# Kernel optimization log

Measured on AMD Instinct MI355X. Metric: run time of the kernel, lower is better.

Reference implementation:

```python
import jax, jax.numpy as jnp
import numpy as np
from jax import lax

B, N, C, NP, NS, H, L = 2, 16384, 256, 2048, 32, 4, 2
DFF = 2 * C
RADIUS = 1.0
EPS = 1e-5


def setup_inputs() -> dict:
    key = jax.random.key(0)
    ks = jax.random.split(key, 12)
    s = 0.02
    f32 = jnp.float32
    return {
        "xyz": jax.random.normal(ks[0], (B, N, 3), f32),
        "features": jax.random.normal(ks[1], (B, C, N), f32),
        # positional encoding: Conv1x1(3->C/2)+BN(eval)+ReLU, Conv1x1(C/2->C)
        "pe1_w": jax.random.normal(ks[2], (C // 2, 3), f32) * s,
        "pe1_b": jnp.zeros((C // 2,), f32),
        "bn_g": jnp.ones((C // 2,), f32),
        "bn_b": jnp.zeros((C // 2,), f32),
        "bn_m": jnp.zeros((C // 2,), f32),
        "bn_v": jnp.ones((C // 2,), f32),
        "pe2_w": jax.random.normal(ks[3], (C, C // 2), f32) * s,
        "pe2_b": jnp.zeros((C,), f32),
        # L pre-norm transformer encoder layers (stacked on leading dim)
        "ipw": jax.random.normal(ks[4], (L, 3 * C, C), f32) * s,
        "ipb": jnp.zeros((L, 3 * C), f32),
        "opw": jax.random.normal(ks[5], (L, C, C), f32) * s,
        "opb": jnp.zeros((L, C), f32),
        "ln1s": jnp.ones((L, C), f32), "ln1b": jnp.zeros((L, C), f32),
        "ln2s": jnp.ones((L, C), f32), "ln2b": jnp.zeros((L, C), f32),
        "fc1w": jax.random.normal(ks[6], (L, DFF, C), f32) * s,
        "fc1b": jnp.zeros((L, DFF), f32),
        "fc2w": jax.random.normal(ks[7], (L, C, DFF), f32) * s,
        "fc2b": jnp.zeros((L, C), f32),
    }


def _fps(xyz, npoint):
    # D-FPS starting from point 0 (pointnet2 convention). xyz: [B,N,3]
    b, n, _ = xyz.shape

    def step(carry, _):
        dists, far = carry
        centroid = jnp.take_along_axis(xyz, far[:, None, None], axis=1)  # [B,1,3]
        d = jnp.sum((xyz - centroid) ** 2, -1)
        dists = jnp.minimum(dists, d)
        return (dists, jnp.argmax(dists, -1).astype(jnp.int32)), far

    init = (jnp.full((b, n), 1e10, jnp.float32), jnp.zeros((b,), jnp.int32))
    _, idx = lax.scan(step, init, None, length=npoint)
    return idx.T  # [B, npoint]


def _ball_query(xyz, new_xyz, radius, ns):
    # first <=ns points within radius, padded with the first hit. [B,NP,NS]
    n = xyz.shape[1]
    d2 = jnp.sum((new_xyz[:, :, None, :] - xyz[:, None, :, :]) ** 2, -1)  # [B,NP,N]
    scores = jnp.where(d2 < radius * radius, jnp.arange(n, dtype=jnp.int32), n)
    svals = jnp.sort(scores, axis=-1)[..., :ns]
    order = jnp.argsort(scores, axis=-1)[..., :ns].astype(jnp.int32)
    valid = svals < n
    return jnp.where(valid, order, order[..., :1])


def _ln(x, s, b):
    m = jnp.mean(x, -1, keepdims=True)
    v = jnp.var(x, -1, keepdims=True)
    return (x - m) * lax.rsqrt(v + EPS) * s + b


def _mha(x, w, bias, ow, ob):
    # x: [S, Bn, D] (seq-first, like nn.MultiheadAttention)
    S, Bn, D = x.shape
    hd = D // H
    qkv = x @ w.T + bias
    q, k, v = jnp.split(qkv, 3, -1)
    rs = lambda t: t.reshape(S, Bn, H, hd).transpose(1, 2, 0, 3)  # [Bn,H,S,hd]
    q, k, v = rs(q), rs(k), rs(v)
    att = jax.nn.softmax(jnp.einsum('bhqd,bhkd->bhqk', q, k) * (1.0 / np.sqrt(hd)), -1)
    o = jnp.einsum('bhqk,bhkd->bhqd', att, v).transpose(2, 0, 1, 3).reshape(S, Bn, D)
    return o @ ow.T + ob


def reference(xyz, features, pe1_w, pe1_b, bn_g, bn_b, bn_m, bn_v, pe2_w, pe2_b,
              ipw, ipb, opw, opb, ln1s, ln1b, ln2s, ln2b, fc1w, fc1b, fc2w, fc2b):
    # --- sample + group ---
    fps_idx = _fps(lax.stop_gradient(xyz), NP)                       # [B,NP]
    new_xyz = jnp.take_along_axis(xyz, fps_idx[:, :, None], axis=1)  # [B,NP,3]
    idx = _ball_query(lax.stop_gradient(xyz), lax.stop_gradient(new_xyz), RADIUS, NS)
    g_xyz = jax.vmap(lambda p, i: p[i])(xyz, idx) - new_xyz[:, :, None, :]  # [B,NP,NS,3]
    g_xyz = g_xyz.transpose(0, 3, 1, 2)                              # [B,3,NP,NS]
    g_feat = jax.vmap(lambda f, i: f[:, i])(features, idx)           # [B,C,NP,NS]
    # --- positional encoding (conv1x1 + BN(eval) + ReLU, conv1x1) ---
    h = jnp.einsum('oc,bcps->bops', pe1_w, g_xyz) + pe1_b[None, :, None, None]
    h = (h - bn_m[None, :, None, None]) * lax.rsqrt(bn_v + EPS)[None, :, None, None]
    h = jax.nn.relu(h * bn_g[None, :, None, None] + bn_b[None, :, None, None])
    pe = jnp.einsum('oc,bcps->bops', pe2_w, h) + pe2_b[None, :, None, None]
    x = g_feat + pe                                                  # [B,C,NP,NS]
    # --- local transformer over each neighborhood (seq len = NS) ---
    x = x.transpose(0, 2, 1, 3).reshape(B * NP, C, NS).transpose(2, 0, 1)  # [NS,B*NP,C]
    for l in range(L):
        x = _ln(x, ln1s[l], ln1b[l])
        x = x + _mha(x, ipw[l], ipb[l], opw[l], opb[l])
        x = _ln(x, ln2s[l], ln2b[l])
        x = x + jax.nn.relu(x @ fc1w[l].T + fc1b[l]) @ fc2w[l].T + fc2b[l]
    tf = x.transpose(1, 2, 0).reshape(B, NP, C, NS).transpose(0, 2, 1, 3)  # [B,C,NP,NS]
    Lf = NP * NS

    def scat(feat_b, tf_b, idx_b):
        idx_f = idx_b.reshape(-1)          # [Lf]
        ff = tf_b.reshape(C, -1)           # [C,Lf]
        pos = jnp.arange(Lf, dtype=jnp.int32)
        first = jax.ops.segment_min(pos, idx_f, num_segments=N)  # [N], maxint if absent
        valid = first < Lf
        safe = jnp.where(valid, first, 0)
        return jnp.where(valid[None, :], ff[:, safe], feat_b)    # [C,N]

    out = jax.vmap(scat)(features, tf, idx)  # [B,C,N]
    return out.transpose(0, 2, 1)            # [B,N,C]
```

## Files before the change

kernel.cpp:

```cpp
#include <hip/hip_runtime.h>

#define NB 2
#define NN 16384
#define NC 256
#define NPp 2048
#define NSs 32
#define NH 4
#define HDh 64
#define NL 2
#define NDFF 512
#define LFv (NPp*NSs)
#define LNEPS 1e-5f
#define NBLK 256
#define NTHR 512

typedef short s16x8 __attribute__((ext_vector_type(8)));
typedef float f32x4 __attribute__((ext_vector_type(4)));
typedef float f32x2 __attribute__((ext_vector_type(2)));
typedef unsigned short u16;
typedef unsigned long long u64;

struct CtlBlock { int prog[2]; int ctr1; int ctr2; int bar; };

__device__ __forceinline__ u16 f2bf(float f){
  unsigned u = __float_as_uint(f);
  u += 0x7fffu + ((u>>16)&1u);
  return (u16)(u>>16);
}

__device__ __forceinline__ f32x4 mfma16(s16x8 a, s16x8 b, f32x4 c){
  return __builtin_amdgcn_mfma_f32_16x16x32_bf16(a, b, c, 0, 0, 0);
}

__device__ __forceinline__ f32x2 pk_add(f32x2 a, f32x2 b){
  f32x2 d; asm("v_pk_add_f32 %0, %1, %2" : "=v"(d) : "v"(a), "v"(b)); return d;
}
__device__ __forceinline__ f32x2 pk_mul(f32x2 a, f32x2 b){
  f32x2 d; asm("v_pk_mul_f32 %0, %1, %2" : "=v"(d) : "v"(a), "v"(b)); return d;
}

#define DPP_FMAX(v, ctrl) do { \
  int _iv = __float_as_int(v); \
  int _sh = __builtin_amdgcn_update_dpp(_iv, _iv, (ctrl), 0xF, 0xF, false); \
  (v) = fmaxf((v), __int_as_float(_sh)); \
} while(0)

#define DPP_IMIN(v, ctrl) do { \
  int _sh = __builtin_amdgcn_update_dpp((v), (v), (ctrl), 0xF, 0xF, false); \
  (v) = (_sh < (v)) ? _sh : (v); \
} while(0)

struct SMem {
  u64  masks[256];
  u64  keybuf[4];
  float xs[32][NC];
  u16  xn[32][264];
  u16  qb[32][776];
  u16  pb[NH][32][40];
  int  idx_sh[32];
  float gx_sh[32][3];
  float wcoord[2][8][4];
  int  misc[16];
  int  win[32];
};

__global__ void k_prep(const float* __restrict__ ipw, const float* __restrict__ opw,
                       const float* __restrict__ fc1w, const float* __restrict__ fc2w,
                       const float* __restrict__ pe2w,
                       const float* __restrict__ bng, const float* __restrict__ bnb,
                       const float* __restrict__ bnm, const float* __restrict__ bnv,
                       u16* ipwb, u16* opwb, u16* fc1wb, u16* fc2wb, u16* pe2wb,
                       float* bnsc, float* bnsh, int* first, CtlBlock* ctl){
  const int i0 = blockIdx.x*blockDim.x + threadIdx.x;
  const int stride = gridDim.x*blockDim.x;
  for (int i=i0; i<NL*768*NC; i+=stride) ipwb[i] = f2bf(ipw[i]);
  for (int i=i0; i<NL*NC*NC; i+=stride)  opwb[i] = f2bf(opw[i]);
  for (int i=i0; i<NL*NDFF*NC; i+=stride) fc1wb[i] = f2bf(fc1w[i]);
  for (int i=i0; i<NL*NC*NDFF; i+=stride) fc2wb[i] = f2bf(fc2w[i]);
  for (int i=i0; i<NC*128; i+=stride)    pe2wb[i] = f2bf(pe2w[i]);
  for (int i=i0; i<NB*NN; i+=stride)     first[i] = LFv;
  for (int i=i0; i<128; i+=stride){
    float sc = bng[i]*rsqrtf(bnv[i]+LNEPS);
    bnsc[i] = sc; bnsh[i] = bnb[i] - bnm[i]*sc;
  }
  if (i0 == 0){
    ctl->prog[0] = -1; ctl->prog[1] = -1;
    ctl->ctr1 = 0; ctl->ctr2 = 0; ctl->bar = 0;
  }
}

__global__ __launch_bounds__(256) void k_featT(const float* __restrict__ feat,
                                               float* __restrict__ featT){
  __shared__ float T[32][33];
  const int b = blockIdx.y;
  const int n0 = blockIdx.x*32;
  const int t = threadIdx.x;
  const int tn = t & 31, tc = t >> 5;
  for (int cb=0; cb<NC; cb+=32){
    #pragma unroll
    for (int i=0;i<32;i+=8)
      T[tc+i][tn] = feat[((size_t)b*NC + cb+tc+i)*NN + n0+tn];
    __syncthreads();
    #pragma unroll
    for (int i=0;i<32;i+=8)
      featT[((size_t)b*NN + n0+tc+i)*NC + cb+tn] = T[tn][tc+i];
    __syncthreads();
  }
}

__device__ void fps_run(int b, const float* __restrict__ xyz,
                        float* __restrict__ newxyz, CtlBlock* ctl, SMem& sm){
#pragma clang fp contract(off)
  const int t = threadIdx.x;
  const int lane = t & 63, wid = t >> 6;
  const float* xb = xyz + (size_t)b*NN*3;
  f32x2 px2[16], py2[16], pz2[16], dd2[16];
  #pragma unroll
  for (int m=0;m<16;m++){
    int i0 = t + (2*m)*NTHR, i1 = t + (2*m+1)*NTHR;
    px2[m] = f32x2{xb[i0*3],   xb[i1*3]};
    py2[m] = f32x2{xb[i0*3+1], xb[i1*3+1]};
    pz2[m] = f32x2{xb[i0*3+2], xb[i1*3+2]};
    dd2[m] = f32x2{1e10f, 1e10f};
  }
  if (t < 4) sm.keybuf[t] = 0ull;
  float wx = xb[0], wy = xb[1], wz = xb[2];
  if (t==0){
    newxyz[(size_t)b*NPp*3+0]=wx;
    newxyz[(size_t)b*NPp*3+1]=wy;
    newxyz[(size_t)b*NPp*3+2]=wz;
    __hip_atomic_store(&ctl->prog[b], 0, __ATOMIC_RELEASE, __HIP_MEMORY_SCOPE_AGENT);
  }
  float ncx=-wx, ncy=-wy, ncz=-wz;
  __syncthreads();
  for (int step=1; step<NPp; ++step){
    const f32x2 ncx2={ncx,ncx}, ncy2={ncy,ncy}, ncz2={ncz,ncz};
    #pragma unroll
    for (int m=0;m<16;m++){
      f32x2 dx = pk_add(px2[m], ncx2);
      f32x2 dy = pk_add(py2[m], ncy2);
      f32x2 dz = pk_add(pz2[m], ncz2);
      f32x2 s  = pk_add(pk_add(pk_mul(dx,dx), pk_mul(dy,dy)), pk_mul(dz,dz));
      f32x2 d  = dd2[m];
      d.x = fminf(d.x, s.x);
      d.y = fminf(d.y, s.y);
      dd2[m] = d;
    }
    float h8[8];
    #pragma unroll
    for (int q=0;q<8;q++)
      h8[q] = fmaxf(fmaxf(dd2[2*q].x, dd2[2*q].y), fmaxf(dd2[2*q+1].x, dd2[2*q+1].y));
    float M = fmaxf(fmaxf(fmaxf(h8[0],h8[1]),fmaxf(h8[2],h8[3])),
                    fmaxf(fmaxf(h8[4],h8[5]),fmaxf(h8[6],h8[7])));
    DPP_FMAX(M, 0x111); DPP_FMAX(M, 0x112); DPP_FMAX(M, 0x114); DPP_FMAX(M, 0x118);
    DPP_FMAX(M, 0x142); DPP_FMAX(M, 0x143);
    const unsigned Mb = (unsigned)__builtin_amdgcn_readlane(__float_as_int(M), 63);
    const float Ms = __int_as_float((int)Mb);
    int li = 0x7fffffff;
    #pragma unroll
    for (int m=15;m>=0;m--){
      if (dd2[m].y == Ms) li = t + (2*m+1)*NTHR;
      if (dd2[m].x == Ms) li = t + (2*m)*NTHR;
    }
    DPP_IMIN(li, 0x111); DPP_IMIN(li, 0x112); DPP_IMIN(li, 0x114); DPP_IMIN(li, 0x118);
    DPP_IMIN(li, 0x142); DPP_IMIN(li, 0x143);
    const int li63 = __builtin_amdgcn_readlane(li, 63);
    const int kb = step & 3, cb = step & 1;
    if (lane==0){
      u64 key = ((u64)Mb << 32) | (unsigned)(0x7fffffff - li63);
      atomicMax(&sm.keybuf[kb], key);
      const float* cp = xb + (size_t)li63*3;
      sm.wcoord[cb][wid][0]=cp[0]; sm.wcoord[cb][wid][1]=cp[1]; sm.wcoord[cb][wid][2]=cp[2];
    }
    __syncthreads();
    const u64 kk = sm.keybuf[kb];
    const int widx = 0x7fffffff - (int)(unsigned)(kk & 0xffffffffu);
    const int wv = (widx & (NTHR-1)) >> 6;
    const float nx = sm.wcoord[cb][wv][0];
    const float ny = sm.wcoord[cb][wv][1];
    const float nz = sm.wcoord[cb][wv][2];
    ncx=-nx; ncy=-ny; ncz=-nz;
    if (t==0){
      newxyz[((size_t)b*NPp+step)*3+0]=nx;
      newxyz[((size_t)b*NPp+step)*3+1]=ny;
      newxyz[((size_t)b*NPp+step)*3+2]=nz;
      sm.keybuf[(step+2)&3] = 0ull;
      if ((step & 7) == 7 || step == NPp-1)
        __hip_atomic_store(&ctl->prog[b], step, __ATOMIC_RELEASE, __HIP_MEMORY_SCOPE_AGENT);
    }
  }
}

__device__ void seq_ballq(const float* __restrict__ xb, float cx, float cy, float cz,
                          SMem& sm, int t, int lane, int wid){
#pragma clang fp contract(off)
  for (int it=0; it<32; ++it){
    int cid = wid*32 + it;
    int i = cid*64 + lane;
    float dx=xb[i*3]-cx, dy=xb[i*3+1]-cy, dz=xb[i*3+2]-cz;
    float d2=(dx*dx+dy*dy)+dz*dz;
    u64 m = __ballot(d2 < 1.0f);
    if (lane==0) sm.masks[cid] = m;
  }
  __syncthreads();
  if (wid==0){
    u64 mk[4]; int cnt=0;
    #pragma unroll
    for (int j=0;j<4;j++){ mk[j]=sm.masks[lane*4+j]; cnt += __popcll(mk[j]); }
    int inc = cnt;
    #pragma unroll
    for (int ofs=1; ofs<64; ofs<<=1){
      int v = __shfl_up(inc, ofs);
      if (lane >= ofs) inc += v;
    }
    int r = inc - cnt;
    int tot = __shfl(inc, 63);
    #pragma unroll
    for (int j=0;j<4;j++){
      u64 msk = mk[j];
      int base = (lane*4+j)*64;
      while (msk && r < NSs){
        int bpos = __ffsll(msk)-1;
        sm.idx_sh[r] = base + bpos;
        msk &= msk-1;
        ++r;
      }
      if (r >= NSs) break;
    }
    int cc = tot < NSs ? tot : NSs;
    int pv = (tot > 0) ? sm.idx_sh[0] : 0;
    if (lane < NSs && lane >= cc) sm.idx_sh[lane] = pv;
  }
  __syncthreads();
}

__device__ __forceinline__ void ln_block512(SMem& sm, const float* __restrict__ s_,
                                            const float* __restrict__ b_, int t){
  const int s = t >> 4, j = t & 15;
  float v[16];
  float sum = 0.f;
  #pragma unroll
  for (int k=0;k<16;k++){ v[k]=sm.xs[s][j*16+k]; sum += v[k]; }
  #pragma unroll
  for (int m=1;m<16;m<<=1) sum += __shfl_xor(sum, m);
  const float mean = sum * (1.f/256.f);
  float vs = 0.f;
  #pragma unroll
  for (int k=0;k<16;k++){ float d=v[k]-mean; vs += d*d; }
  #pragma unroll
  for (int m=1;m<16;m<<=1) vs += __shfl_xor(vs, m);
  const float rstd = rsqrtf(vs*(1.f/256.f) + LNEPS);
  #pragma unroll
  for (int k=0;k<16;k++){
    int c = j*16+k;
    float y = (v[k]-mean)*rstd*s_[c] + b_[c];
    sm.xs[s][c] = y;
    sm.xn[s][c] = f2bf(y);
  }
}

__device__ void seq_pe_tf(SMem& sm, int b, int p,
    const float* __restrict__ xyz, const float* __restrict__ features,
    const float* __restrict__ featT, int useT, const float* __restrict__ newxyz,
    const float* __restrict__ pe1w, const float* __restrict__ pe1b,
    const float* __restrict__ bnsc, const float* __restrict__ bnsh,
    const u16* __restrict__ pe2wb, const float* __restrict__ pe2b,
    const u16* __restrict__ ipwb, const float* __restrict__ ipb,
    const u16* __restrict__ opwb, const float* __restrict__ opb,
    const float* __restrict__ ln1s, const float* __restrict__ ln1b,
    const float* __restrict__ ln2s, const float* __restrict__ ln2b,
    const u16* __restrict__ fc1wb, const float* __restrict__ fc1b,
    const u16* __restrict__ fc2wb, const float* __restrict__ fc2b){
  const int t = threadIdx.x, lane = t & 63, wid = t >> 6;
  const int c15 = lane & 15, g4 = lane >> 4;

  if (t < 96){
    int s = t/3, d = t%3;
    sm.gx_sh[s][d] = xyz[((size_t)b*NN + sm.idx_sh[s])*3 + d] - newxyz[(size_t)p*3 + d];
  }
  if (useT){
    for (int e=t; e<32*NC; e+=NTHR){
      int s=e>>8, c=e&255;
      sm.xs[s][c] = featT[((size_t)b*NN + sm.idx_sh[s])*NC + c];
    }
  } else {
    for (int e=t; e<32*NC; e+=NTHR){
      int s=e>>8, c=e&255;
      sm.xs[s][c] = features[((size_t)b*NC + c)*NN + sm.idx_sh[s]];
    }
  }
  __syncthreads();
  for (int i=t; i<32*128; i+=NTHR){
    int s = i >> 7, o = i & 127;
    float h = pe1w[o*3]*sm.gx_sh[s][0] + pe1w[o*3+1]*sm.gx_sh[s][1] + pe1w[o*3+2]*sm.gx_sh[s][2] + pe1b[o];
    h = h*bnsc[o] + bnsh[o];
    sm.xn[s][o] = f2bf(h > 0.f ? h : 0.f);
  }
  __syncthreads();
  for (int tt=wid; tt<32; tt+=8){
    int m0 = (tt & 1)*16, n0 = (tt >> 1)*16;
    f32x4 acc = {0.f,0.f,0.f,0.f};
    #pragma unroll
    for (int kk=0; kk<4; kk++){
      s16x8 a = *(const s16x8*)&sm.xn[m0+c15][kk*32 + g4*8];
      s16x8 bb = *(const s16x8*)&pe2wb[(size_t)(n0+c15)*128 + kk*32 + g4*8];
      acc = mfma16(a, bb, acc);
    }
    int col = n0 + c15;
    float bias = pe2b[col];
    #pragma unroll
    for (int r=0;r<4;r++) sm.xs[m0 + g4*4 + r][col] += acc[r] + bias;
  }
  __syncthreads();

  for (int l=0; l<NL; ++l){
    ln_block512(sm, ln1s + l*NC, ln1b + l*NC, t);
    __syncthreads();
    const u16* Wq = ipwb + (size_t)l*768*NC;
    const float* bq = ipb + l*768;
    for (int tt=wid; tt<96; tt+=8){
      int m0 = (tt & 1)*16, n0 = (tt >> 1)*16;
      f32x4 acc = {0.f,0.f,0.f,0.f};
      #pragma unroll
      for (int kk=0;kk<8;kk++){
        s16x8 a = *(const s16x8*)&sm.xn[m0+c15][kk*32 + g4*8];
        s16x8 bb = *(const s16x8*)&Wq[(size_t)(n0+c15)*NC + kk*32 + g4*8];
        acc = mfma16(a, bb, acc);
      }
      int col = n0 + c15;
      float bias = bq[col];
      #pragma unroll
      for (int r=0;r<4;r++) sm.qb[m0 + g4*4 + r][col] = f2bf(acc[r] + bias);
    }
    __syncthreads();
    {
      const int h = wid & 3;
      const int mt = wid >> 2;
      f32x4 lac[2];
      #pragma unroll
      for (int nt=0;nt<2;nt++){
        f32x4 acc = {0.f,0.f,0.f,0.f};
        #pragma unroll
        for (int kk=0;kk<2;kk++){
          s16x8 a = *(const s16x8*)&sm.qb[mt*16+c15][h*HDh + kk*32 + g4*8];
          s16x8 bb = *(const s16x8*)&sm.qb[nt*16+c15][256 + h*HDh + kk*32 + g4*8];
          acc = mfma16(a, bb, acc);
        }
        lac[nt] = acc;
      }
      #pragma unroll
      for (int r=0;r<4;r++){
        float v0 = lac[0][r]*0.125f, v1 = lac[1][r]*0.125f;
        float mx = fmaxf(v0, v1);
        #pragma unroll
        for (int m=1;m<16;m<<=1) mx = fmaxf(mx, __shfl_xor(mx, m));
        float e0 = expf(v0-mx), e1 = expf(v1-mx);
        float smm = e0 + e1;
        #pragma unroll
        for (int m=1;m<16;m<<=1) smm += __shfl_xor(smm, m);
        float inv = 1.f/smm;
        int row = mt*16 + g4*4 + r;
        sm.pb[h][row][c15]    = f2bf(e0*inv);
        sm.pb[h][row][16+c15] = f2bf(e1*inv);
      }
      f32x4 oac[4];
      #pragma unroll
      for (int nt=0;nt<4;nt++){
        s16x8 bb;
        #pragma unroll
        for (int e=0;e<8;e++) bb[e] = (short)sm.qb[g4*8+e][512 + h*HDh + nt*16 + c15];
        f32x4 acc = {0.f,0.f,0.f,0.f};
        s16x8 a = *(const s16x8*)&sm.pb[h][mt*16+c15][g4*8];
        oac[nt] = mfma16(a, bb, acc);
      }
      __syncthreads();
      #pragma unroll
      for (int nt=0;nt<4;nt++)
        #pragma unroll
        for (int r=0;r<4;r++)
          sm.xn[mt*16 + g4*4 + r][h*HDh + nt*16 + c15] = f2bf(oac[nt][r]);
    }
    __syncthreads();
    const u16* Wo = opwb + (size_t)l*NC*NC;
    const float* bo = opb + l*NC;
    for (int tt=wid; tt<32; tt+=8){
      int m0 = (tt & 1)*16, n0 = (tt >> 1)*16;
      f32x4 acc = {0.f,0.f,0.f,0.f};
      #pragma unroll
      for (int kk=0;kk<8;kk++){
        s16x8 a = *(const s16x8*)&sm.xn[m0+c15][kk*32 + g4*8];
        s16x8 bb = *(const s16x8*)&Wo[(size_t)(n0+c15)*NC + kk*32 + g4*8];
        acc = mfma16(a, bb, acc);
      }
      int col = n0 + c15;
      float bias = bo[col];
      #pragma unroll
      for (int r=0;r<4;r++) sm.xs[m0 + g4*4 + r][col] += acc[r] + bias;
    }
    __syncthreads();
    ln_block512(sm, ln2s + l*NC, ln2b + l*NC, t);
    __syncthreads();
    const u16* W1 = fc1wb + (size_t)l*NDFF*NC;
    for (int tt=wid; tt<64; tt+=8){
      int m0 = (tt & 1)*16, n0 = (tt >> 1)*16;
      f32x4 acc = {0.f,0.f,0.f,0.f};
      #pragma unroll
      for (int kk=0;kk<8;kk++){
        s16x8 a = *(const s16x8*)&sm.xn[m0+c15][kk*32 + g4*8];
        s16x8 bb = *(const s16x8*)&W1[(size_t)(n0+c15)*NC + kk*32 + g4*8];
        acc = mfma16(a, bb, acc);
      }
      int col = n0 + c15;
      float bias = fc1b[l*NDFF + col];
      #pragma unroll
      for (int r=0;r<4;r++){
        float v = acc[r] + bias;
        sm.qb[m0 + g4*4 + r][col] = f2bf(v > 0.f ? v : 0.f);
      }
    }
    __syncthreads();
    const u16* W2 = fc2wb + (size_t)l*NC*NDFF;
    for (int tt=wid; tt<32; tt+=8){
      int m0 = (tt & 1)*16, n0 = (tt >> 1)*16;
      f32x4 acc = {0.f,0.f,0.f,0.f};
      #pragma unroll
      for (int kk=0;kk<16;kk++){
        s16x8 a = *(const s16x8*)&sm.qb[m0+c15][kk*32 + g4*8];
        s16x8 bb = *(const s16x8*)&W2[(size_t)(n0+c15)*NDFF + kk*32 + g4*8];
        acc = mfma16(a, bb, acc);
      }
      int col = n0 + c15;
      float bias = fc2b[l*NC + col];
      #pragma unroll
      for (int r=0;r<4;r++) sm.xs[m0 + g4*4 + r][col] += acc[r] + bias;
    }
    __syncthreads();
  }
}

__global__ __launch_bounds__(NTHR,1) void k_mega(
    const float* __restrict__ xyz, const float* __restrict__ features,
    const float* __restrict__ featT, int useT,
    float* __restrict__ newxyz, int* __restrict__ first, CtlBlock* ctl,
    const float* __restrict__ pe1w, const float* __restrict__ pe1b,
    const float* __restrict__ bnsc, const float* __restrict__ bnsh,
    const u16* __restrict__ pe2wb, const float* __restrict__ pe2b,
    const u16* __restrict__ ipwb, const float* __restrict__ ipb,
    const u16* __restrict__ opwb, const float* __restrict__ opb,
    const float* __restrict__ ln1s, const float* __restrict__ ln1b,
    const float* __restrict__ ln2s, const float* __restrict__ ln2b,
    const u16* __restrict__ fc1wb, const float* __restrict__ fc1b,
    const u16* __restrict__ fc2wb, const float* __restrict__ fc2b,
    float* __restrict__ out){
  __shared__ SMem sm;
  const int t = threadIdx.x, lane = t & 63, wid = t >> 6;

  if (blockIdx.x < NB){
    fps_run(blockIdx.x, xyz, newxyz, ctl, sm);
  } else {
    for (;;){
      if (t==0) sm.misc[1] = atomicAdd(&ctl->ctr1, 1);
      __syncthreads();
      int p = sm.misc[1];
      if (p >= NB*NPp) break;
      int b = p >> 11, pp = p & (NPp-1);
      if (t==0){
        while (__hip_atomic_load(&ctl->prog[b], __ATOMIC_RELAXED, __HIP_MEMORY_SCOPE_AGENT) < pp)
          __builtin_amdgcn_s_sleep(2);
        __builtin_amdgcn_fence(__ATOMIC_ACQUIRE, "agent");
      }
      __syncthreads();
      float cx = newxyz[(size_t)p*3], cy = newxyz[(size_t)p*3+1], cz = newxyz[(size_t)p*3+2];
      seq_ballq(xyz + (size_t)b*NN*3, cx, cy, cz, sm, t, lane, wid);
      if (t < NSs) atomicMin(&first[b*NN + sm.idx_sh[t]], pp*NSs + t);
      __syncthreads();
    }
  }

  __syncthreads();
  if (t==0){
    __builtin_amdgcn_fence(__ATOMIC_RELEASE, "agent");
    __hip_atomic_fetch_add(&ctl->bar, 1, __ATOMIC_RELAXED, __HIP_MEMORY_SCOPE_AGENT);
    while (__hip_atomic_load(&ctl->bar, __ATOMIC_RELAXED, __HIP_MEMORY_SCOPE_AGENT) < NBLK)
      __builtin_amdgcn_s_sleep(8);
    __builtin_amdgcn_fence(__ATOMIC_ACQUIRE, "agent");
  }
  __syncthreads();

  for (;;){
    if (t==0) sm.misc[1] = atomicAdd(&ctl->ctr2, 1);
    __syncthreads();
    int p = sm.misc[1];
    if (p >= NB*NPp) break;
    int b = p >> 11, pp = p & (NPp-1);
    float cx = newxyz[(size_t)p*3], cy = newxyz[(size_t)p*3+1], cz = newxyz[(size_t)p*3+2];
    seq_ballq(xyz + (size_t)b*NN*3, cx, cy, cz, sm, t, lane, wid);
    if (t==0) sm.misc[2] = 0;
    __syncthreads();
    if (t < NSs){
      int pos = pp*NSs + t;
      int f = __hip_atomic_load(&first[b*NN + sm.idx_sh[t]], __ATOMIC_RELAXED, __HIP_MEMORY_SCOPE_AGENT);
      int w = (f == pos) ? 1 : 0;
      sm.win[t] = w;
      if (w) atomicOr(&sm.misc[2], 1);
    }
    __syncthreads();
    if (!sm.misc[2]) continue;
    seq_pe_tf(sm, b, p, xyz, features, featT, useT, newxyz,
              pe1w, pe1b, bnsc, bnsh, pe2wb, pe2b, ipwb, ipb, opwb, opb,
              ln1s, ln1b, ln2s, ln2b, fc1wb, fc1b, fc2wb, fc2b);
    for (int e=t; e<NSs*NC; e+=NTHR){
      int s = e >> 8, c = e & 255;
      if (sm.win[s]) out[((size_t)b*NN + sm.idx_sh[s])*NC + c] = sm.xs[s][c];
    }
    __syncthreads();
  }
}

__global__ __launch_bounds__(256) void k_outfill_T(const float* __restrict__ featT,
                                                   const int* __restrict__ first,
                                                   float* __restrict__ out){
  const int t = threadIdx.x;
  for (int rr=0; rr<8; ++rr){
    int row = blockIdx.x*8 + rr;
    if (first[row] == LFv)
      out[(size_t)row*NC + t] = featT[(size_t)row*NC + t];
  }
}

__global__ __launch_bounds__(256) void k_outfill_noT(const float* __restrict__ feat,
                                                     const int* __restrict__ first,
                                                     float* __restrict__ out){
  __shared__ float T[32][33];
  const int b = blockIdx.y;
  const int n0 = blockIdx.x*32;
  const int t = threadIdx.x;
  const int tn = t & 31, tc = t >> 5;
  for (int cb=0; cb<NC; cb+=32){
    #pragma unroll
    for (int i=0;i<32;i+=8)
      T[tc+i][tn] = feat[((size_t)b*NC + cb+tc+i)*NN + n0+tn];
    __syncthreads();
    #pragma unroll
    for (int i=0;i<32;i+=8){
      int n = n0 + tc + i;
      if (first[b*NN+n] == LFv)
        out[((size_t)b*NN + n)*NC + cb+tn] = T[tn][tc+i];
    }
    __syncthreads();
  }
}

extern "C" void kernel_launch(void* const* d_in, const int* in_sizes, int n_in,
                              void* d_out, int out_size, void* d_ws, size_t ws_size,
                              hipStream_t stream){
  const float* xyz   = (const float*)d_in[0];
  const float* feat  = (const float*)d_in[1];
  const float* pe1w  = (const float*)d_in[2];
  const float* pe1b  = (const float*)d_in[3];
  const float* bng   = (const float*)d_in[4];
  const float* bnb   = (const float*)d_in[5];
  const float* bnm   = (const float*)d_in[6];
  const float* bnv   = (const float*)d_in[7];
  const float* pe2w  = (const float*)d_in[8];
  const float* pe2b  = (const float*)d_in[9];
  const float* ipw   = (const float*)d_in[10];
  const float* ipb   = (const float*)d_in[11];
  const float* opw   = (const float*)d_in[12];
  const float* opb   = (const float*)d_in[13];
  const float* ln1s  = (const float*)d_in[14];
  const float* ln1b  = (const float*)d_in[15];
  const float* ln2s  = (const float*)d_in[16];
  const float* ln2b  = (const float*)d_in[17];
  const float* fc1w  = (const float*)d_in[18];
  const float* fc1b  = (const float*)d_in[19];
  const float* fc2w  = (const float*)d_in[20];
  const float* fc2b  = (const float*)d_in[21];
  float* out = (float*)d_out;

  char* ws = (char*)d_ws;
  size_t off = 0;
  auto alloc = [&](size_t bytes)->void*{
    void* p = ws + off;
    off = (off + bytes + 255) & ~(size_t)255;
    return p;
  };
  float* newxyz  = (float*)alloc((size_t)NB*NPp*3*4);
  int*   first   = (int*)  alloc((size_t)NB*NN*4);
  CtlBlock* ctl  = (CtlBlock*)alloc(sizeof(CtlBlock));
  float* bnsc    = (float*)alloc(128*4);
  float* bnsh    = (float*)alloc(128*4);
  u16*   ipwb    = (u16*)  alloc((size_t)NL*768*NC*2);
  u16*   opwb    = (u16*)  alloc((size_t)NL*NC*NC*2);
  u16*   fc1wb   = (u16*)  alloc((size_t)NL*NDFF*NC*2);
  u16*   fc2wb   = (u16*)  alloc((size_t)NL*NC*NDFF*2);
  u16*   pe2wb   = (u16*)  alloc((size_t)NC*128*2);
  float* featT   = (float*)(ws + off);
  int useT = (off + (size_t)NB*NN*NC*4 <= ws_size) ? 1 : 0;

  k_prep<<<512, 256, 0, stream>>>(ipw, opw, fc1w, fc2w, pe2w, bng, bnb, bnm, bnv,
                                  ipwb, opwb, fc1wb, fc2wb, pe2wb, bnsc, bnsh, first, ctl);
  if (useT)
    k_featT<<<dim3(NN/32, NB), 256, 0, stream>>>(feat, featT);

  const float* featT_c = featT;
  void* kargs[] = {
    (void*)&xyz, (void*)&feat, (void*)&featT_c, (void*)&useT,
    (void*)&newxyz, (void*)&first, (void*)&ctl,
    (void*)&pe1w, (void*)&pe1b, (void*)&bnsc, (void*)&bnsh,
    (void*)&pe2wb, (void*)&pe2b, (void*)&ipwb, (void*)&ipb,
    (void*)&opwb, (void*)&opb, (void*)&ln1s, (void*)&ln1b,
    (void*)&ln2s, (void*)&ln2b, (void*)&fc1wb, (void*)&fc1b,
    (void*)&fc2wb, (void*)&fc2b, (void*)&out };
  hipLaunchCooperativeKernel((void*)k_mega, dim3(NBLK), dim3(NTHR), kargs, 0, stream);

  if (useT)
    k_outfill_T<<<(NB*NN)/8, 256, 0, stream>>>(featT, first, out);
  else
    k_outfill_noT<<<dim3(NN/32, NB), 256, 0, stream>>>(feat, first, out);
  (void)in_sizes; (void)n_in; (void)out_size;
}
```

Baseline: 4.474 ms.

## Speculatively run neighborhood transformers during FPS and commit winners afterwards

Worker blocks now run the full positional-encoding and transformer pipeline for every neighborhood as soon as its FPS centroid is ready. Each result is stored in a bf16 buffer, and a new commit kernel picks the first-occurrence winner per point or falls back to the input features. This hides the transformer work behind the serial FPS phase instead of running it in a second pass after FPS. The cost is computing every neighborhood rather than only the winners, a large extra workspace, and bf16 rounding of outputs. The FPS step is also reworked: the cross-wave argmax uses per-wave shared-memory keys instead of a shared atomicMax, the winner's coordinates are read from registers, and only indices are stored, with centroid coordinates re-read from xyz.

```diff
diff --git a/kernel.cpp b/kernel.cpp
--- a/kernel.cpp
+++ b/kernel.cpp
@@ -52,14 +52,15 @@
 
 struct SMem {
   u64  masks[256];
-  u64  keybuf[4];
-  float xs[32][NC];
+  u64  wvkey[2][8];
+  float wvc[2][8][4];
+  int  idxbuf[8];
+  float xs[32][260];
   u16  xn[32][264];
   u16  qb[32][776];
   u16  pb[NH][32][40];
   int  idx_sh[32];
   float gx_sh[32][3];
-  float wcoord[2][8][4];
   int  misc[16];
   int  win[32];
 };
@@ -108,8 +109,10 @@
   }
 }
 
-__device__ void fps_run(int b, const float* __restrict__ xyz,
-                        float* __restrict__ newxyz, CtlBlock* ctl, SMem& sm){
+#define SELC(S) case S: scx = px2[(S)>>1][(S)&1]; scy = py2[(S)>>1][(S)&1]; scz = pz2[(S)>>1][(S)&1]; break;
+
+__device__ void fps_run(int b, const float* __restrict__ xyz, int* __restrict__ fps_idx,
+                        CtlBlock* ctl, SMem& sm){
 #pragma clang fp contract(off)
   const int t = threadIdx.x;
   const int lane = t & 63, wid = t >> 6;
@@ -123,15 +126,15 @@
     pz2[m] = f32x2{xb[i0*3+2], xb[i1*3+2]};
     dd2[m] = f32x2{1e10f, 1e10f};
   }
-  if (t < 4) sm.keybuf[t] = 0ull;
-  float wx = xb[0], wy = xb[1], wz = xb[2];
-  if (t==0){
-    newxyz[(size_t)b*NPp*3+0]=wx;
-    newxyz[(size_t)b*NPp*3+1]=wy;
-    newxyz[(size_t)b*NPp*3+2]=wz;
-    __hip_atomic_store(&ctl->prog[b], 0, __ATOMIC_RELEASE, __HIP_MEMORY_SCOPE_AGENT);
-  }
-  float ncx=-wx, ncy=-wy, ncz=-wz;
+  float ncx, ncy, ncz;
+  {
+    float wx = xb[0], wy = xb[1], wz = xb[2];
+    ncx=-wx; ncy=-wy; ncz=-wz;
+    if (t==0){
+      fps_idx[b*NPp] = 0;
+      __hip_atomic_store(&ctl->prog[b], 0, __ATOMIC_RELEASE, __HIP_MEMORY_SCOPE_AGENT);
+    }
+  }
   __syncthreads();
   for (int step=1; step<NPp; ++step){
     const f32x2 ncx2={ncx,ncx}, ncy2={ncy,ncy}, ncz2={ncz,ncz};
@@ -154,8 +157,8 @@
                     fmaxf(fmaxf(h8[4],h8[5]),fmaxf(h8[6],h8[7])));
     DPP_FMAX(M, 0x111); DPP_FMAX(M, 0x112); DPP_FMAX(M, 0x114); DPP_FMAX(M, 0x118);
     DPP_FMAX(M, 0x142); DPP_FMAX(M, 0x143);
-    const unsigned Mb = (unsigned)__builtin_amdgcn_readlane(__float_as_int(M), 63);
-    const float Ms = __int_as_float((int)Mb);
+    const int Mi = __builtin_amdgcn_readlane(__float_as_int(M), 63);
+    const float Ms = __int_as_float(Mi);
     int li = 0x7fffffff;
     #pragma unroll
     for (int m=15;m>=0;m--){
@@ -164,29 +167,45 @@
     }
     DPP_IMIN(li, 0x111); DPP_IMIN(li, 0x112); DPP_IMIN(li, 0x114); DPP_IMIN(li, 0x118);
     DPP_IMIN(li, 0x142); DPP_IMIN(li, 0x143);
-    const int li63 = __builtin_amdgcn_readlane(li, 63);
-    const int kb = step & 3, cb = step & 1;
-    if (lane==0){
-      u64 key = ((u64)Mb << 32) | (unsigned)(0x7fffffff - li63);
-      atomicMax(&sm.keybuf[kb], key);
-      const float* cp = xb + (size_t)li63*3;
-      sm.wcoord[cb][wid][0]=cp[0]; sm.wcoord[cb][wid][1]=cp[1]; sm.wcoord[cb][wid][2]=cp[2];
-    }
-    __syncthreads();
-    const u64 kk = sm.keybuf[kb];
-    const int widx = 0x7fffffff - (int)(unsigned)(kk & 0xffffffffu);
-    const int wv = (widx & (NTHR-1)) >> 6;
-    const float nx = sm.wcoord[cb][wv][0];
-    const float ny = sm.wcoord[cb][wv][1];
-    const float nz = sm.wcoord[cb][wv][2];
-    ncx=-nx; ncy=-ny; ncz=-nz;
+    const int liw = __builtin_amdgcn_readlane(li, 63);
+    const int sb = step & 1;
+    if (lane==0)
+      sm.wvkey[sb][wid] = ((u64)(unsigned)Mi << 32) | (unsigned)(0x7fffffff - liw);
+    {
+      const int slot = liw >> 9;
+      float scx=0.f, scy=0.f, scz=0.f;
+      switch(slot){
+        SELC(0) SELC(1) SELC(2) SELC(3) SELC(4) SELC(5) SELC(6) SELC(7)
+        SELC(8) SELC(9) SELC(10) SELC(11) SELC(12) SELC(13) SELC(14) SELC(15)
+        SELC(16) SELC(17) SELC(18) SELC(19) SELC(20) SELC(21) SELC(22) SELC(23)
+        SELC(24) SELC(25) SELC(26) SELC(27) SELC(28) SELC(29) SELC(30) SELC(31)
+        default: break;
+      }
+      if (t == (liw & (NTHR-1))){
+        sm.wvc[sb][wid][0]=scx; sm.wvc[sb][wid][1]=scy; sm.wvc[sb][wid][2]=scz;
+      }
+    }
+    __syncthreads();
+    u64 bk = sm.wvkey[sb][0];
+    float bx=sm.wvc[sb][0][0], by=sm.wvc[sb][0][1], bz=sm.wvc[sb][0][2];
+    #pragma unroll
+    for (int w=1;w<8;w++){
+      u64 k2 = sm.wvkey[sb][w];
+      if (k2 > bk){ bk=k2; bx=sm.wvc[sb][w][0]; by=sm.wvc[sb][w][1]; bz=sm.wvc[sb][w][2]; }
+    }
+    ncx=-bx; ncy=-by; ncz=-bz;
     if (t==0){
-      newxyz[((size_t)b*NPp+step)*3+0]=nx;
-      newxyz[((size_t)b*NPp+step)*3+1]=ny;
-      newxyz[((size_t)b*NPp+step)*3+2]=nz;
-      sm.keybuf[(step+2)&3] = 0ull;
-      if ((step & 7) == 7 || step == NPp-1)
+      int widx = 0x7fffffff - (int)(unsigned)(bk & 0xffffffffu);
+      sm.idxbuf[step & 7] = widx;
+      if ((step & 7) == 7){
+        int s0 = step - 7;
+        #pragma unroll
+        for (int j=0;j<8;j++){
+          int s = s0 + j;
+          if (s > 0) fps_idx[b*NPp + s] = sm.idxbuf[s & 7];
+        }
         __hip_atomic_store(&ctl->prog[b], step, __ATOMIC_RELEASE, __HIP_MEMORY_SCOPE_AGENT);
+      }
     }
   }
 }
@@ -259,9 +278,9 @@
   }
 }
 
-__device__ void seq_pe_tf(SMem& sm, int b, int p,
+__device__ void seq_pe_tf(SMem& sm, int b, float ccx, float ccy, float ccz,
     const float* __restrict__ xyz, const float* __restrict__ features,
-    const float* __restrict__ featT, int useT, const float* __restrict__ newxyz,
+    const float* __restrict__ featT, int useT,
     const float* __restrict__ pe1w, const float* __restrict__ pe1b,
     const float* __restrict__ bnsc, const float* __restrict__ bnsh,
     const u16* __restrict__ pe2wb, const float* __restrict__ pe2b,
@@ -276,7 +295,8 @@
 
   if (t < 96){
     int s = t/3, d = t%3;
-    sm.gx_sh[s][d] = xyz[((size_t)b*NN + sm.idx_sh[s])*3 + d] - newxyz[(size_t)p*3 + d];
+    float cd = (d==0) ? ccx : ((d==1) ? ccy : ccz);
+    sm.gx_sh[s][d] = xyz[((size_t)b*NN + sm.idx_sh[s])*3 + d] - cd;
   }
   if (useT){
     for (int e=t; e<32*NC; e+=NTHR){
@@ -440,8 +460,8 @@
 
 __global__ __launch_bounds__(NTHR,1) void k_mega(
     const float* __restrict__ xyz, const float* __restrict__ features,
-    const float* __restrict__ featT, int useT,
-    float* __restrict__ newxyz, int* __restrict__ first, CtlBlock* ctl,
+    const float* __restrict__ featT, int useT, u16* __restrict__ tfb, int spec,
+    int* __restrict__ fps_idx, int* __restrict__ first, CtlBlock* ctl,
     const float* __restrict__ pe1w, const float* __restrict__ pe1b,
     const float* __restrict__ bnsc, const float* __restrict__ bnsh,
     const u16* __restrict__ pe2wb, const float* __restrict__ pe2b,
@@ -456,7 +476,7 @@
   const int t = threadIdx.x, lane = t & 63, wid = t >> 6;
 
   if (blockIdx.x < NB){
-    fps_run(blockIdx.x, xyz, newxyz, ctl, sm);
+    fps_run(blockIdx.x, xyz, fps_idx, ctl, sm);
   } else {
     for (;;){
       if (t==0) sm.misc[1] = atomicAdd(&ctl->ctr1, 1);
@@ -468,14 +488,26 @@
         while (__hip_atomic_load(&ctl->prog[b], __ATOMIC_RELAXED, __HIP_MEMORY_SCOPE_AGENT) < pp)
           __builtin_amdgcn_s_sleep(2);
         __builtin_amdgcn_fence(__ATOMIC_ACQUIRE, "agent");
+        sm.misc[4] = fps_idx[p];
       }
       __syncthreads();
-      float cx = newxyz[(size_t)p*3], cy = newxyz[(size_t)p*3+1], cz = newxyz[(size_t)p*3+2];
+      int ci = sm.misc[4];
+      float cx = xyz[((size_t)b*NN + ci)*3];
+      float cy = xyz[((size_t)b*NN + ci)*3+1];
+      float cz = xyz[((size_t)b*NN + ci)*3+2];
       seq_ballq(xyz + (size_t)b*NN*3, cx, cy, cz, sm, t, lane, wid);
       if (t < NSs) atomicMin(&first[b*NN + sm.idx_sh[t]], pp*NSs + t);
+      if (spec){
+        seq_pe_tf(sm, b, cx, cy, cz, xyz, features, featT, useT,
+                  pe1w, pe1b, bnsc, bnsh, pe2wb, pe2b, ipwb, ipb, opwb, opb,
+                  ln1s, ln1b, ln2s, ln2b, fc1wb, fc1b, fc2wb, fc2b);
+        for (int e=t; e<NSs*NC; e+=NTHR)
+          tfb[(size_t)p*NSs*NC + e] = f2bf(sm.xs[e>>8][e&255]);
+      }
       __syncthreads();
     }
   }
+  if (spec) return;
 
   __syncthreads();
   if (t==0){
@@ -486,14 +518,16 @@
     __builtin_amdgcn_fence(__ATOMIC_ACQUIRE, "agent");
   }
   __syncthreads();
-
   for (;;){
     if (t==0) sm.misc[1] = atomicAdd(&ctl->ctr2, 1);
     __syncthreads();
     int p = sm.misc[1];
     if (p >= NB*NPp) break;
     int b = p >> 11, pp = p & (NPp-1);
-    float cx = newxyz[(size_t)p*3], cy = newxyz[(size_t)p*3+1], cz = newxyz[(size_t)p*3+2];
+    int ci = fps_idx[p];
+    float cx = xyz[((size_t)b*NN + ci)*3];
+    float cy = xyz[((size_t)b*NN + ci)*3+1];
+    float cz = xyz[((size_t)b*NN + ci)*3+2];
     seq_ballq(xyz + (size_t)b*NN*3, cx, cy, cz, sm, t, lane, wid);
     if (t==0) sm.misc[2] = 0;
     __syncthreads();
@@ -506,7 +540,7 @@
     }
     __syncthreads();
     if (!sm.misc[2]) continue;
-    seq_pe_tf(sm, b, p, xyz, features, featT, useT, newxyz,
+    seq_pe_tf(sm, b, cx, cy, cz, xyz, features, featT, useT,
               pe1w, pe1b, bnsc, bnsh, pe2wb, pe2b, ipwb, ipb, opwb, opb,
               ln1s, ln1b, ln2s, ln2b, fc1wb, fc1b, fc2wb, fc2b);
     for (int e=t; e<NSs*NC; e+=NTHR){
@@ -514,6 +548,31 @@
       if (sm.win[s]) out[((size_t)b*NN + sm.idx_sh[s])*NC + c] = sm.xs[s][c];
     }
     __syncthreads();
+  }
+}
+
+__global__ __launch_bounds__(256) void k_commit(const u16* __restrict__ tfb,
+                                                const int* __restrict__ first,
+                                                const float* __restrict__ featT,
+                                                const float* __restrict__ feat,
+                                                int useT, float* __restrict__ out){
+  const int t = threadIdx.x;
+  const int row0 = blockIdx.x*16;
+  for (int r=0;r<16;++r){
+    int row = row0 + r;
+    int b = row >> 14;
+    int f = first[row];
+    float v;
+    if (f != LFv){
+      unsigned u = tfb[((size_t)b*NPp*NSs + f)*NC + t];
+      v = __int_as_float((int)(u << 16));
+    } else if (useT){
+      v = featT[(size_t)row*NC + t];
+    } else {
+      int n = row & (NN-1);
+      v = feat[((size_t)b*NC + t)*NN + n];
+    }
+    out[(size_t)row*NC + t] = v;
   }
 }
 
@@ -585,7 +644,7 @@
     off = (off + bytes + 255) & ~(size_t)255;
     return p;
   };
-  float* newxyz  = (float*)alloc((size_t)NB*NPp*3*4);
+  int*   fps_idx = (int*)  alloc((size_t)NB*NPp*4);
   int*   first   = (int*)  alloc((size_t)NB*NN*4);
   CtlBlock* ctl  = (CtlBlock*)alloc(sizeof(CtlBlock));
   float* bnsc    = (float*)alloc(128*4);
@@ -595,8 +654,10 @@
   u16*   fc1wb   = (u16*)  alloc((size_t)NL*NDFF*NC*2);
   u16*   fc2wb   = (u16*)  alloc((size_t)NL*NC*NDFF*2);
   u16*   pe2wb   = (u16*)  alloc((size_t)NC*128*2);
-  float* featT   = (float*)(ws + off);
   int useT = (off + (size_t)NB*NN*NC*4 <= ws_size) ? 1 : 0;
+  float* featT = (float*)(useT ? alloc((size_t)NB*NN*NC*4) : (void*)ws);
+  int spec = (off + (size_t)NB*NPp*NSs*NC*2 <= ws_size) ? 1 : 0;
+  u16* tfb = (u16*)(spec ? alloc((size_t)NB*NPp*NSs*NC*2) : (void*)ws);
 
   k_prep<<<512, 256, 0, stream>>>(ipw, opw, fc1w, fc2w, pe2w, bng, bnb, bnm, bnv,
                                   ipwb, opwb, fc1wb, fc2wb, pe2wb, bnsc, bnsh, first, ctl);
@@ -605,8 +666,8 @@
 
   const float* featT_c = featT;
   void* kargs[] = {
-    (void*)&xyz, (void*)&feat, (void*)&featT_c, (void*)&useT,
-    (void*)&newxyz, (void*)&first, (void*)&ctl,
+    (void*)&xyz, (void*)&feat, (void*)&featT_c, (void*)&useT, (void*)&tfb, (void*)&spec,
+    (void*)&fps_idx, (void*)&first, (void*)&ctl,
     (void*)&pe1w, (void*)&pe1b, (void*)&bnsc, (void*)&bnsh,
     (void*)&pe2wb, (void*)&pe2b, (void*)&ipwb, (void*)&ipb,
     (void*)&opwb, (void*)&opb, (void*)&ln1s, (void*)&ln1b,
@@ -614,9 +675,12 @@
     (void*)&fc2wb, (void*)&fc2b, (void*)&out };
   hipLaunchCooperativeKernel((void*)k_mega, dim3(NBLK), dim3(NTHR), kargs, 0, stream);
 
-  if (useT)
+  if (spec){
+    k_commit<<<(NB*NN)/16, 256, 0, stream>>>(tfb, first, featT, feat, useT, out);
+  } else if (useT){
     k_outfill_T<<<(NB*NN)/8, 256, 0, stream>>>(featT, first, out);
-  else
+  } else {
     k_outfill_noT<<<dim3(NN/32, NB), 256, 0, stream>>>(feat, first, out);
+  }
   (void)in_sizes; (void)n_in; (void)out_size;
 }
```

Result: slower. 5.295 ms (+18.4%).
